# Optimization experiments

Hardware: AMD Instinct MI355X
Metric: run time of the kernel (lower is better)

Reference implementation:

```python
import math
import jax, jax.numpy as jnp
import numpy as np

NUM_HEADS = 16
TAU_RCS, LAMBDA_RCS = 2.0, 0.6
PATCH = 16
PREFIX = 8
GAUSS_STD = 5.0


def gaussian_window(d1, d2, std):
    c = 1.0 / (std * math.sqrt(2.0))
    k1 = (jnp.arange(d1, dtype=jnp.float32) - (d1 - 1) / 2.0) * c
    k2 = (jnp.arange(d2, dtype=jnp.float32) - (d2 - 1) / 2.0) * c
    return jnp.exp(-(k1[:, None] ** 2 + k2[None, :] ** 2))  # [d1, d2]


def attention_addition(d1, d2, prefix, std):
    # out[(a,b),(c,d)] = window[a-c+d1-1, b-d+d2-1]  (conv of delta images with window)
    win = gaussian_window(2 * d1 - 1, 2 * d2 - 1, std)
    ia = jnp.arange(d1)
    jb = jnp.arange(d2)
    r = ia[:, None] - ia[None, :] + (d1 - 1)   # [d1, d1]
    s = jb[:, None] - jb[None, :] + (d2 - 1)   # [d2, d2]
    add = win[r[:, None, :, None], s[None, :, None, :]]  # [d1,d2,d1,d2]
    add = add.reshape(d1 * d2, d1 * d2)
    add = jnp.pad(add, ((prefix, 0), (prefix, 0)))  # zero rows/cols for prefix tokens
    return add[None]  # [1, N, N]


def setup_inputs() -> dict:
    key = jax.random.key(0)
    ks = jax.random.split(key, 5)
    B, C = 4, 1024
    d1 = d2 = 512 // PATCH  # 32
    N = d1 * d2 + PREFIX    # 1032
    H = NUM_HEADS
    x = jax.random.normal(ks[0], (B, N, C), dtype=jnp.float32)
    qkv_w = jax.random.normal(ks[1], (3 * C, C), dtype=jnp.float32) * 0.02
    qkv_b = jnp.zeros((3 * C,), dtype=jnp.float32)
    proj_w = jax.random.normal(ks[2], (C, C), dtype=jnp.float32) * 0.02
    proj_b = jnp.zeros((C,), dtype=jnp.float32)
    attn_add = attention_addition(d1, d2, PREFIX, GAUSS_STD)
    # stored RCS attention maps are softmax outputs -> row-normalized positives
    rcs = jax.random.uniform(ks[3], (B * H, N, N), dtype=jnp.float32)
    rcs = rcs / jnp.sum(rcs, axis=-1, keepdims=True)
    return {"x": x, "qkv_w": qkv_w, "qkv_b": qkv_b, "proj_w": proj_w,
            "proj_b": proj_b, "attn_addition": attn_add, "rcs_attn": rcs}


def reference(x, qkv_w, qkv_b, proj_w, proj_b, attn_addition, rcs_attn):
    B, N, C = x.shape
    H = NUM_HEADS
    hd = C // H
    scale = hd ** -0.5
    qkv = jnp.einsum('bnc,dc->bnd', x, qkv_w) + qkv_b  # [B,N,3C]
    q, k, v = jnp.split(qkv, 3, axis=-1)
    def to_heads(t):
        return t.reshape(B, N, H, hd).transpose(0, 2, 1, 3).reshape(B * H, N, hd)
    k = to_heads(k)
    v = to_heads(v)
    # custom K-K attention with additive Gaussian bias
    attn = jnp.einsum('bnd,bmd->bnm', k, k) * scale + attn_addition
    attn = jax.nn.softmax(attn, axis=-1)
    # RCS blending with stored intermediate attention maps
    attn = TAU_RCS * ((1.0 - LAMBDA_RCS) * attn + LAMBDA_RCS * rcs_attn)
    out = jnp.einsum('bnm,bmd->bnd', attn, v)  # [B*H, N, hd]
    out = out.reshape(B, H, N, hd).transpose(0, 2, 1, 3).reshape(B, N, C)
    out = jnp.einsum('bnc,dc->bnd', out, proj_w) + proj_b
    return out
```

## Files before the change

### kernel.cpp

```cpp
#include <hip/hip_runtime.h>
#include <stdint.h>

#define NSEQ 1032
#define CDIM 1024
#define HD 64
#define H_HEADS 16
#define BROWS 4128
#define SCALE 0.125f

typedef __attribute__((ext_vector_type(8))) short bf16x8;
typedef __attribute__((ext_vector_type(4))) float f32x4;

__device__ __forceinline__ unsigned short f2bf(float f) {
  union { float f; uint32_t u; } c; c.f = f;
  uint32_t u = c.u;
  return (unsigned short)((u + 0x7fffu + ((u >> 16) & 1u)) >> 16);
}

__device__ __forceinline__ void gl16(const void* gp, void* lp) {
  __builtin_amdgcn_global_load_lds((const __attribute__((address_space(1))) void*)gp,
                                   (__attribute__((address_space(3))) void*)lp, 16, 0, 0);
}

__global__ void convert_f32_bf16(const float* __restrict__ src, unsigned short* __restrict__ dst, int n4) {
  int i = blockIdx.x * blockDim.x + threadIdx.x;
  if (i >= n4) return;
  float4 v = ((const float4*)src)[i];
  ushort4 o;
  o.x = f2bf(v.x); o.y = f2bf(v.y); o.z = f2bf(v.z); o.w = f2bf(v.w);
  ((ushort4*)dst)[i] = o;
}

template<int MODE>
__global__ __launch_bounds__(256, 2) void gemm_bt(
    const unsigned short* __restrict__ A,
    const unsigned short* __restrict__ Bw,
    const float* __restrict__ bias,
    unsigned short* __restrict__ outK,
    unsigned short* __restrict__ outV,
    float* __restrict__ outF,
    int M, int K)
{
  __shared__ unsigned short As[128 * 32];
  __shared__ unsigned short Bs[128 * 32];
  const int t = threadIdx.x;
  const int w = t >> 6, lane = t & 63, lr = lane & 15, lg = lane >> 4;
  const int wr = w >> 1, wc = w & 1;
  const int m0 = blockIdx.y * 128, n0 = blockIdx.x * 128;
  f32x4 acc[4][4] = {};

  for (int ks = 0; ks < K; ks += 32) {
    #pragma unroll
    for (int q = 0; q < 2; ++q) {
      const int o = t + (q << 8);
      const int row = o >> 2, kc = o & 3;
      int ra = m0 + row; ra = ra < M ? ra : M - 1;
      gl16(A + (size_t)ra * K + ks + kc * 8, (void*)(As + o * 8));
      gl16(Bw + (size_t)(n0 + row) * K + ks + kc * 8, (void*)(Bs + o * 8));
    }
    __syncthreads();
    bf16x8 af[4], bfr[4];
    #pragma unroll
    for (int m = 0; m < 4; ++m)
      af[m] = *(const bf16x8*)(As + (wr * 64 + m * 16 + lr) * 32 + lg * 8);
    #pragma unroll
    for (int n = 0; n < 4; ++n)
      bfr[n] = *(const bf16x8*)(Bs + (wc * 64 + n * 16 + lr) * 32 + lg * 8);
    #pragma unroll
    for (int m = 0; m < 4; ++m)
      #pragma unroll
      for (int n = 0; n < 4; ++n)
        acc[m][n] = __builtin_amdgcn_mfma_f32_16x16x32_bf16(af[m], bfr[n], acc[m][n], 0, 0, 0);
    __syncthreads();
  }

  #pragma unroll
  for (int m = 0; m < 4; ++m) {
    const int rowb = m0 + wr * 64 + m * 16 + lg * 4;
    #pragma unroll
    for (int n = 0; n < 4; ++n) {
      const int col = n0 + wc * 64 + n * 16 + lr;
      const float bv = bias[col];
      #pragma unroll
      for (int r = 0; r < 4; ++r) {
        const int row = rowb + r;
        if (row >= M) continue;
        const float v = acc[m][n][r] + bv;
        if (MODE == 0) {
          const int b = row / NSEQ, nn = row - b * NSEQ;
          if (col < CDIM) {
            const int h = col >> 6, d = col & 63;
            outK[((size_t)(b * H_HEADS + h) * NSEQ + nn) * HD + d] = f2bf(v);
          } else {
            const int jj = col - CDIM, h = jj >> 6, d = jj & 63;
            outV[((size_t)(b * H_HEADS + h) * HD + d) * NSEQ + nn] = f2bf(v);
          }
        } else {
          outF[(size_t)row * CDIM + col] = v;
        }
      }
    }
  }
}

__global__ __launch_bounds__(256, 2) void attn_fused(
    const unsigned short* __restrict__ Kb,
    const unsigned short* __restrict__ Vt,
    const float* __restrict__ rcs,
    unsigned short* __restrict__ outp)
{
  __shared__ unsigned short Kc[2][64 * 72];
  __shared__ unsigned short Vs[2][64 * 72];
  __shared__ unsigned short Ps[64 * 72];
  __shared__ __align__(16) float As[2][64 * 64];
  const int t = threadIdx.x;
  const int w = t >> 6, lane = t & 63, lr = lane & 15, lg = lane >> 4;
  const int bid = blockIdx.x;
  const int nb = (bid & 7) * 136 + (bid >> 3);
  const int bh = nb / 17, rt = nb - bh * 17;
  const int i_base = rt * 64 + w * 16;
  const int arow = w * 16 + lr;
  const float* rbase = rcs + (size_t)bh * NSEQ * NSEQ;
  const unsigned short* kbase = Kb + (size_t)bh * NSEQ * HD;
  const unsigned short* vbase = Vt + (size_t)bh * HD * NSEQ;

  bf16x8 akr[2];
  {
    int row = i_base + lr; if (row > NSEQ - 1) row = NSEQ - 1;
    const unsigned short* p = kbase + (size_t)row * HD + lg * 8;
    akr[0] = *(const bf16x8*)(p);
    akr[1] = *(const bf16x8*)(p + 32);
  }

  const int irow_base = i_base + lg * 4;
  int i1v[4], j1v[4]; float iokf[4];
  #pragma unroll
  for (int r = 0; r < 4; ++r) {
    const int irow = irow_base + r;
    const int ip = irow - 8;
    i1v[r] = ip >> 5; j1v[r] = ip & 31;
    iokf[r] = (irow >= 8) ? 1.f : 0.f;
  }

  f32x4 accP[4] = {};
  f32x4 accR[4] = {};
  float lsum[4] = {0.f, 0.f, 0.f, 0.f};

  {
    #pragma unroll
    for (int q = 0; q < 2; ++q) {
      const int o = t + (q << 8);
      const int row = o >> 3, ch = o & 7;
      int mrow = row; if (mrow > NSEQ - 1) mrow = NSEQ - 1;
      bf16x8 kv = *(const bf16x8*)(kbase + (size_t)mrow * HD + ch * 8);
      *(bf16x8*)(Kc[0] + row * 72 + ch * 8) = kv;
      int cb = ch * 8; if (cb + 8 > NSEQ) cb = NSEQ - 8;
      bf16x8 vv = *(const bf16x8*)(vbase + (size_t)row * NSEQ + cb);
      *(bf16x8*)(Vs[0] + row * 72 + ch * 8) = vv;
    }
    #pragma unroll
    for (int q = 0; q < 4; ++q) {
      const int p = t + (q << 8);
      const int row = p >> 4, sch = p & 15;
      const int gch = (sch & 8) | ((sch ^ row) & 7);
      int grow = rt * 64 + row; if (grow > NSEQ - 1) grow = NSEQ - 1;
      int gcol = gch * 4; if (gcol > NSEQ - 4) gcol = NSEQ - 4;
      gl16(rbase + (size_t)grow * NSEQ + gcol, (void*)(As[0] + p * 4));
    }
    __syncthreads();
  }

  for (int mt = 0; mt < 17; ++mt) {
    const int mB = mt * 64;
    const int cur = mt & 1, nxt = cur ^ 1;

    bf16x8 kreg[2], vreg[2];
    if (mt < 16) {
      const int nB = mB + 64;
      #pragma unroll
      for (int q = 0; q < 2; ++q) {
        const int o = t + (q << 8);
        const int row = o >> 3, ch = o & 7;
        int mrow = nB + row; if (mrow > NSEQ - 1) mrow = NSEQ - 1;
        kreg[q] = *(const bf16x8*)(kbase + (size_t)mrow * HD + ch * 8);
        int cb = nB + ch * 8; if (cb + 8 > NSEQ) cb = NSEQ - 8;
        vreg[q] = *(const bf16x8*)(vbase + (size_t)row * NSEQ + cb);
      }
      #pragma unroll
      for (int q = 0; q < 4; ++q) {
        const int p = t + (q << 8);
        const int row = p >> 4, sch = p & 15;
        const int gch = (sch & 8) | ((sch ^ row) & 7);
        int grow = rt * 64 + row; if (grow > NSEQ - 1) grow = NSEQ - 1;
        int gcol = nB + gch * 4; if (gcol > NSEQ - 4) gcol = NSEQ - 4;
        gl16(rbase + (size_t)grow * NSEQ + gcol, (void*)(As[nxt] + p * 4));
      }
    }

    f32x4 s[4];
    #pragma unroll
    for (int fn = 0; fn < 4; ++fn) {
      f32x4 z = {0.f, 0.f, 0.f, 0.f};
      bf16x8 b0 = *(const bf16x8*)(Kc[cur] + (16 * fn + lr) * 72 + lg * 8);
      bf16x8 b1 = *(const bf16x8*)(Kc[cur] + (16 * fn + lr) * 72 + 32 + lg * 8);
      z = __builtin_amdgcn_mfma_f32_16x16x32_bf16(akr[0], b0, z, 0, 0, 0);
      z = __builtin_amdgcn_mfma_f32_16x16x32_bf16(akr[1], b1, z, 0, 0, 0);
      s[fn] = z;
    }

    #pragma unroll
    for (int fn = 0; fn < 4; ++fn) {
      const int mcol = mB + 16 * fn + lr;
      const int mp = mcol - 8;
      const int m1 = mp >> 5, m2 = mp & 31;
      const float mokf = (mcol >= 8 && mcol < NSEQ) ? 1.f : 0.f;
      const bool mlt = (mcol < NSEQ);
      #pragma unroll
      for (int r = 0; r < 4; ++r) {
        const int di = i1v[r] - m1, dj = j1v[r] - m2;
        const float ad = __expf(-0.02f * (float)(di * di + dj * dj)) * iokf[r] * mokf;
        const float sv = s[fn][r] * SCALE + ad;
        const float p = mlt ? __expf(sv) : 0.f;
        lsum[r] += p;
        Ps[(w * 16 + lg * 4 + r) * 72 + 16 * fn + lr] = f2bf(p);
      }
    }

    bf16x8 af[2];
    #pragma unroll
    for (int kf = 0; kf < 2; ++kf) {
      bf16x8 a;
      const int kg = mB + kf * 32 + lg * 8;
      if (kg + 8 <= NSEQ) {
        const float* ab = As[cur] + arow * 64;
        const int c0 = kf * 8 + 2 * lg;
        const int s0 = (c0 & 8) | ((c0 ^ arow) & 7);
        const int s1 = (c0 & 8) | (((c0 + 1) ^ arow) & 7);
        f32x4 lo = *(const f32x4*)(ab + s0 * 4);
        f32x4 hi = *(const f32x4*)(ab + s1 * 4);
        a[0] = (short)f2bf(lo[0]); a[1] = (short)f2bf(lo[1]);
        a[2] = (short)f2bf(lo[2]); a[3] = (short)f2bf(lo[3]);
        a[4] = (short)f2bf(hi[0]); a[5] = (short)f2bf(hi[1]);
        a[6] = (short)f2bf(hi[2]); a[7] = (short)f2bf(hi[3]);
      } else {
        #pragma unroll
        for (int j = 0; j < 8; ++j) a[j] = 0;
      }
      af[kf] = a;
    }

    bf16x8 pa0 = *(const bf16x8*)(Ps + (w * 16 + lr) * 72 + lg * 8);
    bf16x8 pa1 = *(const bf16x8*)(Ps + (w * 16 + lr) * 72 + 32 + lg * 8);
    #pragma unroll
    for (int fd = 0; fd < 4; ++fd) {
      bf16x8 v0 = *(const bf16x8*)(Vs[cur] + (16 * fd + lr) * 72 + lg * 8);
      bf16x8 v1 = *(const bf16x8*)(Vs[cur] + (16 * fd + lr) * 72 + 32 + lg * 8);
      accP[fd] = __builtin_amdgcn_mfma_f32_16x16x32_bf16(pa0, v0, accP[fd], 0, 0, 0);
      accP[fd] = __builtin_amdgcn_mfma_f32_16x16x32_bf16(pa1, v1, accP[fd], 0, 0, 0);
      accR[fd] = __builtin_amdgcn_mfma_f32_16x16x32_bf16(af[0], v0, accR[fd], 0, 0, 0);
      accR[fd] = __builtin_amdgcn_mfma_f32_16x16x32_bf16(af[1], v1, accR[fd], 0, 0, 0);
    }

    if (mt < 16) {
      #pragma unroll
      for (int q = 0; q < 2; ++q) {
        const int o = t + (q << 8);
        const int row = o >> 3, ch = o & 7;
        *(bf16x8*)(Kc[nxt] + row * 72 + ch * 8) = kreg[q];
        *(bf16x8*)(Vs[nxt] + row * 72 + ch * 8) = vreg[q];
      }
    }
    __syncthreads();
  }

  #pragma unroll
  for (int r = 0; r < 4; ++r) {
    float v = lsum[r];
    v += __shfl_xor(v, 1); v += __shfl_xor(v, 2);
    v += __shfl_xor(v, 4); v += __shfl_xor(v, 8);
    lsum[r] = v;
  }

  const int b = bh >> 4, hh = bh & 15;
  #pragma unroll
  for (int fd = 0; fd < 4; ++fd) {
    #pragma unroll
    for (int r = 0; r < 4; ++r) {
      const int irow = i_base + lg * 4 + r;
      if (irow < NSEQ) {
        const float val = 0.8f * accP[fd][r] / lsum[r] + 1.2f * accR[fd][r];
        outp[(size_t)(b * NSEQ + irow) * CDIM + hh * 64 + 16 * fd + lr] = f2bf(val);
      }
    }
  }
}

extern "C" void kernel_launch(void* const* d_in, const int* in_sizes, int n_in,
                              void* d_out, int out_size, void* d_ws, size_t ws_size,
                              hipStream_t stream) {
  (void)in_sizes; (void)n_in; (void)out_size; (void)ws_size;
  const float* x      = (const float*)d_in[0];
  const float* qkv_w  = (const float*)d_in[1];
  const float* qkv_b  = (const float*)d_in[2];
  const float* proj_w = (const float*)d_in[3];
  const float* proj_b = (const float*)d_in[4];
  const float* rcs    = (const float*)d_in[6];
  float* out = (float*)d_out;

  char* ws = (char*)d_ws;
  unsigned short* x_bf = (unsigned short*)ws; ws += (size_t)BROWS * CDIM * 2;
  unsigned short* wkv  = (unsigned short*)ws; ws += (size_t)2048 * CDIM * 2;
  unsigned short* wp   = (unsigned short*)ws; ws += (size_t)1024 * CDIM * 2;
  unsigned short* Kb   = (unsigned short*)ws; ws += (size_t)64 * NSEQ * HD * 2;
  unsigned short* Vt   = (unsigned short*)ws; ws += (size_t)64 * HD * NSEQ * 2;
  unsigned short* op   = (unsigned short*)ws; ws += (size_t)BROWS * CDIM * 2;

  const int n1 = BROWS * CDIM / 4, n2 = 2048 * CDIM / 4, n3 = 1024 * CDIM / 4;
  convert_f32_bf16<<<(n1 + 255) / 256, 256, 0, stream>>>(x, x_bf, n1);
  convert_f32_bf16<<<(n2 + 255) / 256, 256, 0, stream>>>(qkv_w + 1024 * 1024, wkv, n2);
  convert_f32_bf16<<<(n3 + 255) / 256, 256, 0, stream>>>(proj_w, wp, n3);

  gemm_bt<0><<<dim3(16, 33), 256, 0, stream>>>(x_bf, wkv, qkv_b + 1024, Kb, Vt, nullptr, BROWS, CDIM);
  attn_fused<<<1088, 256, 0, stream>>>(Kb, Vt, rcs, op);
  gemm_bt<1><<<dim3(8, 33), 256, 0, stream>>>(op, wp, proj_b, nullptr, nullptr, out, BROWS, CDIM);
}
```

Before: 211.7 us.

## Stage K and V tiles via direct global-to-LDS loads with XOR swizzle

K and V tiles, like the RCS tile, are now loaded with global_load_lds straight into shared memory instead of going through registers and a later LDS store. They use an XOR-swizzled 64-wide layout in place of 72-element padding. The loop now waits with explicit vmcnt counts so the next tile's loads can stay in flight across the barrier while the current tile is computed. This removes register staging and the store phase, and lowers register pressure and LDS footprint, but relies on hand-counted vmcnt values being correct.

```diff
diff --git a/kernel.cpp b/kernel.cpp
--- a/kernel.cpp
+++ b/kernel.cpp
@@ -109,10 +109,10 @@
     const float* __restrict__ rcs,
     unsigned short* __restrict__ outp)
 {
-  __shared__ unsigned short Kc[2][64 * 72];
-  __shared__ unsigned short Vs[2][64 * 72];
+  __shared__ __align__(16) unsigned short Kc[2][64 * 64];
+  __shared__ __align__(16) unsigned short Vs[2][64 * 64];
+  __shared__ __align__(16) float As[2][64 * 64];
   __shared__ unsigned short Ps[64 * 72];
-  __shared__ __align__(16) float As[2][64 * 64];
   const int t = threadIdx.x;
   const int w = t >> 6, lane = t & 63, lr = lane & 15, lg = lane >> 4;
   const int bid = blockIdx.x;
@@ -124,6 +124,35 @@
   const unsigned short* kbase = Kb + (size_t)bh * NSEQ * HD;
   const unsigned short* vbase = Vt + (size_t)bh * HD * NSEQ;
 
+  auto stage = [&](int tile, int buf) {
+    const int tB = tile * 64;
+    #pragma unroll
+    for (int q = 0; q < 2; ++q) {
+      const int p = t + (q << 8);
+      const int row = p >> 3, sch = p & 7;
+      const int gch = (sch ^ row) & 7;
+      int mrow = tB + row; if (mrow > NSEQ - 1) mrow = NSEQ - 1;
+      gl16(kbase + (size_t)mrow * HD + gch * 8, (void*)(Kc[buf] + p * 8));
+    }
+    #pragma unroll
+    for (int q = 0; q < 2; ++q) {
+      const int p = t + (q << 8);
+      const int row = p >> 3, sch = p & 7;
+      const int gch = (sch ^ row) & 7;
+      int gc = tB + gch * 8; if (gc > NSEQ - 8) gc = NSEQ - 8;
+      gl16(vbase + (size_t)row * NSEQ + gc, (void*)(Vs[buf] + p * 8));
+    }
+    #pragma unroll
+    for (int q = 0; q < 4; ++q) {
+      const int p = t + (q << 8);
+      const int row = p >> 4, sch = p & 15;
+      const int gch = (sch & 8) | ((sch ^ row) & 7);
+      int grow = rt * 64 + row; if (grow > NSEQ - 1) grow = NSEQ - 1;
+      int gcol = tB + gch * 4; if (gcol > NSEQ - 4) gcol = NSEQ - 4;
+      gl16(rbase + (size_t)grow * NSEQ + gcol, (void*)(As[buf] + p * 4));
+    }
+  };
+
   bf16x8 akr[2];
   {
     int row = i_base + lr; if (row > NSEQ - 1) row = NSEQ - 1;
@@ -146,63 +175,33 @@
   f32x4 accR[4] = {};
   float lsum[4] = {0.f, 0.f, 0.f, 0.f};
 
-  {
-    #pragma unroll
-    for (int q = 0; q < 2; ++q) {
-      const int o = t + (q << 8);
-      const int row = o >> 3, ch = o & 7;
-      int mrow = row; if (mrow > NSEQ - 1) mrow = NSEQ - 1;
-      bf16x8 kv = *(const bf16x8*)(kbase + (size_t)mrow * HD + ch * 8);
-      *(bf16x8*)(Kc[0] + row * 72 + ch * 8) = kv;
-      int cb = ch * 8; if (cb + 8 > NSEQ) cb = NSEQ - 8;
-      bf16x8 vv = *(const bf16x8*)(vbase + (size_t)row * NSEQ + cb);
-      *(bf16x8*)(Vs[0] + row * 72 + ch * 8) = vv;
-    }
-    #pragma unroll
-    for (int q = 0; q < 4; ++q) {
-      const int p = t + (q << 8);
-      const int row = p >> 4, sch = p & 15;
-      const int gch = (sch & 8) | ((sch ^ row) & 7);
-      int grow = rt * 64 + row; if (grow > NSEQ - 1) grow = NSEQ - 1;
-      int gcol = gch * 4; if (gcol > NSEQ - 4) gcol = NSEQ - 4;
-      gl16(rbase + (size_t)grow * NSEQ + gcol, (void*)(As[0] + p * 4));
-    }
-    __syncthreads();
-  }
+  stage(0, 0);
 
   for (int mt = 0; mt < 17; ++mt) {
     const int mB = mt * 64;
     const int cur = mt & 1, nxt = cur ^ 1;
 
-    bf16x8 kreg[2], vreg[2];
     if (mt < 16) {
-      const int nB = mB + 64;
-      #pragma unroll
-      for (int q = 0; q < 2; ++q) {
-        const int o = t + (q << 8);
-        const int row = o >> 3, ch = o & 7;
-        int mrow = nB + row; if (mrow > NSEQ - 1) mrow = NSEQ - 1;
-        kreg[q] = *(const bf16x8*)(kbase + (size_t)mrow * HD + ch * 8);
-        int cb = nB + ch * 8; if (cb + 8 > NSEQ) cb = NSEQ - 8;
-        vreg[q] = *(const bf16x8*)(vbase + (size_t)row * NSEQ + cb);
-      }
-      #pragma unroll
-      for (int q = 0; q < 4; ++q) {
-        const int p = t + (q << 8);
-        const int row = p >> 4, sch = p & 15;
-        const int gch = (sch & 8) | ((sch ^ row) & 7);
-        int grow = rt * 64 + row; if (grow > NSEQ - 1) grow = NSEQ - 1;
-        int gcol = nB + gch * 4; if (gcol > NSEQ - 4) gcol = NSEQ - 4;
-        gl16(rbase + (size_t)grow * NSEQ + gcol, (void*)(As[nxt] + p * 4));
-      }
-    }
+      stage(mt + 1, nxt);
+      asm volatile("s_waitcnt vmcnt(8)");
+    } else {
+      asm volatile("s_waitcnt vmcnt(0)");
+    }
+    __builtin_amdgcn_sched_barrier(0);
+    __builtin_amdgcn_s_barrier();
+    __builtin_amdgcn_sched_barrier(0);
+
+    const unsigned short* kc = Kc[cur];
+    const unsigned short* vsb = Vs[cur];
 
     f32x4 s[4];
     #pragma unroll
     for (int fn = 0; fn < 4; ++fn) {
+      const int row = 16 * fn + lr;
+      const int r7 = row & 7;
       f32x4 z = {0.f, 0.f, 0.f, 0.f};
-      bf16x8 b0 = *(const bf16x8*)(Kc[cur] + (16 * fn + lr) * 72 + lg * 8);
-      bf16x8 b1 = *(const bf16x8*)(Kc[cur] + (16 * fn + lr) * 72 + 32 + lg * 8);
+      bf16x8 b0 = *(const bf16x8*)(kc + row * 64 + ((lg ^ r7) & 7) * 8);
+      bf16x8 b1 = *(const bf16x8*)(kc + row * 64 + (((4 + lg) ^ r7) & 7) * 8);
       z = __builtin_amdgcn_mfma_f32_16x16x32_bf16(akr[0], b0, z, 0, 0, 0);
       z = __builtin_amdgcn_mfma_f32_16x16x32_bf16(akr[1], b1, z, 0, 0, 0);
       s[fn] = z;
@@ -253,24 +252,19 @@
     bf16x8 pa1 = *(const bf16x8*)(Ps + (w * 16 + lr) * 72 + 32 + lg * 8);
     #pragma unroll
     for (int fd = 0; fd < 4; ++fd) {
-      bf16x8 v0 = *(const bf16x8*)(Vs[cur] + (16 * fd + lr) * 72 + lg * 8);
-      bf16x8 v1 = *(const bf16x8*)(Vs[cur] + (16 * fd + lr) * 72 + 32 + lg * 8);
+      const int row = 16 * fd + lr;
+      const int r7 = row & 7;
+      bf16x8 v0 = *(const bf16x8*)(vsb + row * 64 + ((lg ^ r7) & 7) * 8);
+      bf16x8 v1 = *(const bf16x8*)(vsb + row * 64 + (((4 + lg) ^ r7) & 7) * 8);
       accP[fd] = __builtin_amdgcn_mfma_f32_16x16x32_bf16(pa0, v0, accP[fd], 0, 0, 0);
       accP[fd] = __builtin_amdgcn_mfma_f32_16x16x32_bf16(pa1, v1, accP[fd], 0, 0, 0);
       accR[fd] = __builtin_amdgcn_mfma_f32_16x16x32_bf16(af[0], v0, accR[fd], 0, 0, 0);
       accR[fd] = __builtin_amdgcn_mfma_f32_16x16x32_bf16(af[1], v1, accR[fd], 0, 0, 0);
     }
 
-    if (mt < 16) {
-      #pragma unroll
-      for (int q = 0; q < 2; ++q) {
-        const int o = t + (q << 8);
-        const int row = o >> 3, ch = o & 7;
-        *(bf16x8*)(Kc[nxt] + row * 72 + ch * 8) = kreg[q];
-        *(bf16x8*)(Vs[nxt] + row * 72 + ch * 8) = vreg[q];
-      }
-    }
-    __syncthreads();
+    __builtin_amdgcn_sched_barrier(0);
+    __builtin_amdgcn_s_barrier();
+    __builtin_amdgcn_sched_barrier(0);
   }
 
   #pragma unroll
```

New measurement: 199.0 us. -6.0%, faster.
